# Kernel optimization log

Hardware: AMD Instinct MI355X
Metric: run time of the kernel (lower is better)

Reference implementation:

```python
import jax, jax.numpy as jnp
import numpy as np

DIM = 1024
HEADS = 16
DIM_HEAD = 64
INNER = HEADS * DIM_HEAD  # 1024
EPS = 1e-5


def setup_inputs() -> dict:
    key = jax.random.key(0)
    ks = jax.random.split(key, 5)
    x = jax.random.normal(ks[0], (4, 2048, DIM), dtype=jnp.float32)
    ln_gamma = jnp.ones((DIM,), dtype=jnp.float32)
    ln_beta = jnp.zeros((DIM,), dtype=jnp.float32)
    # nn.Linear weights ~ U(-1/sqrt(fan_in), 1/sqrt(fan_in)); stored as (out, in) in torch,
    # here kept as (in, out) for x @ W.
    lim = 1.0 / np.sqrt(DIM)
    w_qkv = jax.random.uniform(ks[1], (DIM, 3 * INNER), minval=-lim, maxval=lim, dtype=jnp.float32)
    lim2 = 1.0 / np.sqrt(INNER)
    w_out = jax.random.uniform(ks[2], (INNER, DIM), minval=-lim2, maxval=lim2, dtype=jnp.float32)
    return {"x": x, "ln_gamma": ln_gamma, "ln_beta": ln_beta, "w_qkv": w_qkv, "w_out": w_out}


def reference(x, ln_gamma, ln_beta, w_qkv, w_out):
    b, n, d = x.shape
    # LayerNorm
    mu = jnp.mean(x, axis=-1, keepdims=True)
    var = jnp.mean(jnp.square(x - mu), axis=-1, keepdims=True)
    xn = (x - mu) * jax.lax.rsqrt(var + EPS) * ln_gamma + ln_beta
    # QKV projection
    qkv = xn @ w_qkv  # (b, n, 3*inner)
    q, k, v = jnp.split(qkv, 3, axis=-1)
    def to_heads(t):
        return t.reshape(b, n, HEADS, DIM_HEAD).transpose(0, 2, 1, 3)  # (b,h,n,dh)
    q, k, v = to_heads(q), to_heads(k), to_heads(v)
    scale = DIM_HEAD ** -0.5
    scores = jnp.einsum('bhqd,bhkd->bhqk', q, k) * scale
    causal = jnp.tril(jnp.ones((n, n), dtype=bool))
    scores = jnp.where(causal, scores, -jnp.inf)
    probs = jax.nn.softmax(scores, axis=-1)
    out = jnp.einsum('bhqk,bhkd->bhqd', probs, v)
    out = out.transpose(0, 2, 1, 3).reshape(b, n, INNER)
    return out @ w_out
```

## Files before the change

kernel.cpp:

```cpp
#include <hip/hip_runtime.h>
#include <hip/hip_bf16.h>

#define DIM 1024
#define HEADS 16
#define DH 64
#define SEQ 2048
#define BATCH 4
#define ROWS (BATCH * SEQ)
#define NQKV (3 * DIM)

typedef __attribute__((ext_vector_type(8))) __bf16 bf16x8;
typedef __attribute__((ext_vector_type(4))) __bf16 bf16x4;
typedef __attribute__((ext_vector_type(4))) float f32x4;

__device__ inline void gload16(const void* g, void* l) {
  __builtin_amdgcn_global_load_lds(
      (const __attribute__((address_space(1))) void*)g,
      (__attribute__((address_space(3))) void*)l, 16, 0, 0);
}

__device__ inline float fast_exp2(float x) {
#if __has_builtin(__builtin_amdgcn_exp2f)
  return __builtin_amdgcn_exp2f(x);
#else
  return exp2f(x);
#endif
}

__global__ __launch_bounds__(256) void ln_kernel(
    const float* __restrict__ x, const float* __restrict__ gamma,
    const float* __restrict__ beta, __bf16* __restrict__ xnb) {
  const int row = blockIdx.x;
  const int tid = threadIdx.x;
  const float4* xr = (const float4*)(x + (size_t)row * DIM);
  float4 v = xr[tid];
  float s1 = v.x + v.y + v.z + v.w;
  float s2 = v.x * v.x + v.y * v.y + v.z * v.z + v.w * v.w;
#pragma unroll
  for (int d = 32; d > 0; d >>= 1) {
    s1 += __shfl_xor(s1, d);
    s2 += __shfl_xor(s2, d);
  }
  __shared__ float red1[4], red2[4];
  const int wave = tid >> 6, lane = tid & 63;
  if (lane == 0) { red1[wave] = s1; red2[wave] = s2; }
  __syncthreads();
  s1 = red1[0] + red1[1] + red1[2] + red1[3];
  s2 = red2[0] + red2[1] + red2[2] + red2[3];
  const float mean = s1 * (1.0f / DIM);
  const float var = s2 * (1.0f / DIM) - mean * mean;
  const float rstd = rsqrtf(var + 1e-5f);
  float4 g = ((const float4*)gamma)[tid];
  float4 b = ((const float4*)beta)[tid];
  bf16x4 o;
  o[0] = (__bf16)((v.x - mean) * rstd * g.x + b.x);
  o[1] = (__bf16)((v.y - mean) * rstd * g.y + b.y);
  o[2] = (__bf16)((v.z - mean) * rstd * g.z + b.z);
  o[3] = (__bf16)((v.w - mean) * rstd * g.w + b.w);
  *(bf16x4*)(xnb + (size_t)row * DIM + tid * 4) = o;
}

__global__ __launch_bounds__(256) void transpose_cast(
    const float* __restrict__ in, __bf16* __restrict__ outT, int rows, int cols) {
  __shared__ float tile[32][33];
  const int tx = threadIdx.x & 31, ty = threadIdx.x >> 5;
  const int c0 = blockIdx.x * 32, r0 = blockIdx.y * 32;
#pragma unroll
  for (int rr = ty; rr < 32; rr += 8)
    tile[rr][tx] = in[(size_t)(r0 + rr) * cols + c0 + tx];
  __syncthreads();
#pragma unroll
  for (int rr = ty; rr < 32; rr += 8)
    outT[(size_t)(c0 + rr) * rows + r0 + tx] = (__bf16)tile[tx][rr];
}

template <int MODE>
__global__ __launch_bounds__(256) void gemm128(
    const __bf16* __restrict__ A, const __bf16* __restrict__ Bt, int K, int N,
    float* __restrict__ Cout, __bf16* __restrict__ qb, __bf16* __restrict__ kb,
    __bf16* __restrict__ vtb) {
  __shared__ __bf16 As[2][128 * 32];
  __shared__ __bf16 Bs[2][128 * 32];
  const int tid = threadIdx.x;
  const int wave = tid >> 6, lane = tid & 63;
  const int quad = lane >> 4, l16 = lane & 15;
  const int wm = wave >> 1, wn = wave & 1;
  const size_t tileM = (size_t)blockIdx.x * 128;
  const size_t tileN = (size_t)blockIdx.y * 128;
  const int sel = (MODE == 1) ? (int)(tileN >> 10) : 0;
  const bool vmode = (MODE == 1) && (sel == 2);

  f32x4 acc[4][4];
#pragma unroll
  for (int i = 0; i < 4; ++i)
#pragma unroll
    for (int j = 0; j < 4; ++j) acc[i][j] = (f32x4){0.f, 0.f, 0.f, 0.f};

  const int sr = lane >> 2;
  const int sc = lane & 3;
  const int ck = (l16 >> 1) & 3;

  const __bf16* Abase = A + tileM * (size_t)K;
  const __bf16* Bbase = Bt + tileN * (size_t)K;

  auto stage = [&](int buf, int k0) {
#pragma unroll
    for (int p = 0; p < 2; ++p) {
      const int rbase = p * 64 + wave * 16;
      const int row = rbase + sr;
      const int gc = (sc ^ ((row >> 1) & 3)) << 3;
      gload16(Abase + (size_t)row * K + k0 + gc, &As[buf][rbase * 32]);
      gload16(Bbase + (size_t)row * K + k0 + gc, &Bs[buf][rbase * 32]);
    }
  };

  const int NIT = K >> 5;
  stage(0, 0);
  for (int it = 0; it < NIT; ++it) {
    __syncthreads();
    if (it + 1 < NIT) stage((it + 1) & 1, (it + 1) << 5);
    const int buf = it & 1;
    bf16x8 af[4], bfr[4];
#pragma unroll
    for (int mt = 0; mt < 4; ++mt)
      af[mt] =
          *(const bf16x8*)&As[buf][(wm * 64 + mt * 16 + l16) * 32 + ((quad ^ ck) << 3)];
#pragma unroll
    for (int nt = 0; nt < 4; ++nt)
      bfr[nt] =
          *(const bf16x8*)&Bs[buf][(wn * 64 + nt * 16 + l16) * 32 + ((quad ^ ck) << 3)];
    if (vmode) {
#pragma unroll
      for (int mt = 0; mt < 4; ++mt)
#pragma unroll
        for (int nt = 0; nt < 4; ++nt)
          acc[mt][nt] = __builtin_amdgcn_mfma_f32_16x16x32_bf16(af[mt], bfr[nt],
                                                                acc[mt][nt], 0, 0, 0);
    } else {
#pragma unroll
      for (int mt = 0; mt < 4; ++mt)
#pragma unroll
        for (int nt = 0; nt < 4; ++nt)
          acc[mt][nt] = __builtin_amdgcn_mfma_f32_16x16x32_bf16(bfr[nt], af[mt],
                                                                acc[mt][nt], 0, 0, 0);
    }
  }

  if (MODE == 0) {
#pragma unroll
    for (int mt = 0; mt < 4; ++mt) {
      const size_t m = tileM + wm * 64 + mt * 16 + l16;
#pragma unroll
      for (int nt = 0; nt < 4; ++nt) {
        const size_t n0 = tileN + wn * 64 + nt * 16 + quad * 4;
        *(f32x4*)&Cout[m * (size_t)N + n0] = acc[mt][nt];
      }
    }
  } else if (sel < 2) {
    __bf16* dst = (sel == 0) ? qb : kb;
#pragma unroll
    for (int mt = 0; mt < 4; ++mt) {
      const size_t m = tileM + wm * 64 + mt * 16 + l16;
      const int b = (int)(m >> 11), seq = (int)(m & 2047);
#pragma unroll
      for (int nt = 0; nt < 4; ++nt) {
        const int c = (int)(tileN & 1023) + wn * 64 + nt * 16 + quad * 4;
        const int head = c >> 6, dh = c & 63;
        bf16x4 pk;
#pragma unroll
        for (int r = 0; r < 4; ++r) pk[r] = (__bf16)acc[mt][nt][r];
        *(bf16x4*)&dst[(((size_t)b * HEADS + head) * SEQ + seq) * DH + dh] = pk;
      }
    }
  } else {
#pragma unroll
    for (int nt = 0; nt < 4; ++nt) {
      const int c = (int)(tileN & 1023) + wn * 64 + nt * 16 + l16;
      const int head = c >> 6, dh = c & 63;
#pragma unroll
      for (int mt = 0; mt < 4; ++mt) {
        const size_t m0 = tileM + wm * 64 + mt * 16 + quad * 4;
        const int b = (int)(m0 >> 11), seq = (int)(m0 & 2047);
        bf16x4 pk;
#pragma unroll
        for (int r = 0; r < 4; ++r) pk[r] = (__bf16)acc[mt][nt][r];
        *(bf16x4*)&vtb[(((size_t)b * HEADS + head) * DH + dh) * SEQ + seq] = pk;
      }
    }
  }
}

__global__ __launch_bounds__(256) void attn_kernel(
    const __bf16* __restrict__ qb, const __bf16* __restrict__ kb,
    const __bf16* __restrict__ vtb, __bf16* __restrict__ ob) {
  const int bh = blockIdx.x;
  const int bx = blockIdx.y;
  const int tid = threadIdx.x;
  const int wave = tid >> 6, lane = tid & 63;
  const int quad = lane >> 4, l16 = lane & 15;

  __shared__ __bf16 Ks[2][128 * 64];
  __shared__ __bf16 Vs[2][64 * 128];
  __shared__ __bf16 Ps[4][32 * 36];

  const __bf16* kg = kb + (size_t)bh * SEQ * DH;
  const __bf16* vg = vtb + (size_t)bh * DH * SEQ;

  const int i1 = bx, i2 = 15 - bx;
  const int T = 17;

  const int kr = lane >> 3, kc = lane & 7;
  const int vr = lane >> 4, vc = lane & 15;

  auto stage = [&](int buf, int j) {
#pragma unroll
    for (int p = 0; p < 4; ++p) {
      const int rbase = p * 32 + wave * 8;
      const int row = rbase + kr;
      gload16(kg + (size_t)(j * 128 + row) * DH + ((kc ^ (row & 7)) << 3),
              &Ks[buf][rbase * 64]);
    }
#pragma unroll
    for (int p = 0; p < 4; ++p) {
      const int rbase = p * 16 + wave * 4;
      const int row = rbase + vr;
      gload16(vg + (size_t)row * SEQ + j * 128 + ((vc ^ (row & 7)) << 3),
              &Vs[buf][rbase * 128]);
    }
  };

  const float QSCALE = 0.125f * 1.44269504088896f;
  bf16x8 qf[2][2];
  auto load_q = [&](int i) {
    const __bf16* qbase = qb + ((size_t)bh * SEQ + (size_t)i * 128 + wave * 32) * DH;
#pragma unroll
    for (int mt = 0; mt < 2; ++mt)
#pragma unroll
      for (int ks = 0; ks < 2; ++ks) {
        bf16x8 v = *(const bf16x8*)(qbase + (mt * 16 + l16) * DH + ks * 32 + quad * 8);
#pragma unroll
        for (int e = 0; e < 8; ++e) v[e] = (__bf16)((float)v[e] * QSCALE);
        qf[mt][ks] = v;
      }
  };

  float m_i[2], l_i[2];
  f32x4 o_acc[4][2];
  auto reset_state = [&]() {
#pragma unroll
    for (int mt = 0; mt < 2; ++mt) { m_i[mt] = -1e30f; l_i[mt] = 0.f; }
#pragma unroll
    for (int md = 0; md < 4; ++md)
#pragma unroll
      for (int mt = 0; mt < 2; ++mt) o_acc[md][mt] = (f32x4){0.f, 0.f, 0.f, 0.f};
  };
  const int b_out = bh >> 4, h_out = bh & 15;
  auto epilogue = [&](int i) {
#pragma unroll
    for (int mt = 0; mt < 2; ++mt) {
      float lsum = l_i[mt];
      lsum += __shfl_xor(lsum, 16);
      lsum += __shfl_xor(lsum, 32);
      const float inv = __builtin_amdgcn_rcpf(lsum);
      const int seq = i * 128 + wave * 32 + mt * 16 + l16;
      __bf16* dst = ob + ((size_t)b_out * SEQ + seq) * DIM + h_out * DH;
#pragma unroll
      for (int md = 0; md < 4; ++md) {
        bf16x4 pk;
#pragma unroll
        for (int r = 0; r < 4; ++r) pk[r] = (__bf16)(o_acc[md][mt][r] * inv);
        *(bf16x4*)(dst + md * 16 + quad * 4) = pk;
      }
    }
  };

  load_q(i1);
  reset_state();
  stage(0, 0);

  for (int t = 0; t < T; ++t) {
    __syncthreads();
    if (t + 1 < T) {
      const int jn = (t + 1 <= bx) ? (t + 1) : (t - bx);
      stage((t + 1) & 1, jn);
    }
    const int buf = t & 1;
    const int i = (t <= bx) ? i1 : i2;
    const int j = (t <= bx) ? t : (t - bx - 1);
    const bool diag = (j == i);

    f32x4 sa[8][2];
#pragma unroll
    for (int nt = 0; nt < 8; ++nt)
#pragma unroll
      for (int mt = 0; mt < 2; ++mt) sa[nt][mt] = (f32x4){0.f, 0.f, 0.f, 0.f};
#pragma unroll
    for (int nt = 0; nt < 8; ++nt)
#pragma unroll
      for (int ks = 0; ks < 2; ++ks) {
        bf16x8 kf = *(const bf16x8*)&Ks[buf][(nt * 16 + l16) * 64 +
                                            (((ks * 4 + quad) ^ (l16 & 7)) << 3)];
#pragma unroll
        for (int mt = 0; mt < 2; ++mt)
          sa[nt][mt] =
              __builtin_amdgcn_mfma_f32_16x16x32_bf16(kf, qf[mt][ks], sa[nt][mt], 0, 0, 0);
      }

    if (diag) {
#pragma unroll
      for (int nt = 0; nt < 8; ++nt)
#pragma unroll
        for (int mt = 0; mt < 2; ++mt) {
          const int qrow = wave * 32 + mt * 16 + l16;
#pragma unroll
          for (int r = 0; r < 4; ++r) {
            const int kv = nt * 16 + quad * 4 + r;
            if (kv > qrow) sa[nt][mt][r] = -1e30f;
          }
        }
    }

    float alpha[2];
#pragma unroll
    for (int mt = 0; mt < 2; ++mt) {
      float mx = -1e30f;
#pragma unroll
      for (int nt = 0; nt < 8; ++nt)
#pragma unroll
        for (int r = 0; r < 4; ++r) mx = fmaxf(mx, sa[nt][mt][r]);
      mx = fmaxf(mx, __shfl_xor(mx, 16));
      mx = fmaxf(mx, __shfl_xor(mx, 32));
      const float mnew = fmaxf(m_i[mt], mx);
      alpha[mt] = fast_exp2(m_i[mt] - mnew);
      m_i[mt] = mnew;
      float rs = 0.f;
#pragma unroll
      for (int nt = 0; nt < 8; ++nt)
#pragma unroll
        for (int r = 0; r < 4; ++r) {
          const float p = fast_exp2(sa[nt][mt][r] - mnew);
          sa[nt][mt][r] = p;
          rs += p;
        }
      l_i[mt] = l_i[mt] * alpha[mt] + rs;
    }
#pragma unroll
    for (int md = 0; md < 4; ++md)
#pragma unroll
      for (int mt = 0; mt < 2; ++mt)
#pragma unroll
        for (int r = 0; r < 4; ++r) o_acc[md][mt][r] *= alpha[mt];

#pragma unroll
    for (int c = 0; c < 4; ++c) {
#pragma unroll
      for (int mt = 0; mt < 2; ++mt)
#pragma unroll
        for (int ntl = 0; ntl < 2; ++ntl) {
          const int nt = c * 2 + ntl;
          bf16x4 pk;
#pragma unroll
          for (int r = 0; r < 4; ++r) pk[r] = (__bf16)sa[nt][mt][r];
          *(bf16x4*)&Ps[wave][(mt * 16 + l16) * 36 + ntl * 16 + quad * 4] = pk;
        }
      bf16x8 pf[2];
#pragma unroll
      for (int mt = 0; mt < 2; ++mt)
        pf[mt] = *(const bf16x8*)&Ps[wave][(mt * 16 + l16) * 36 + quad * 8];
#pragma unroll
      for (int md = 0; md < 4; ++md) {
        bf16x8 vf = *(const bf16x8*)&Vs[buf][(md * 16 + l16) * 128 +
                                            (((c * 4 + quad) ^ (l16 & 7)) << 3)];
#pragma unroll
        for (int mt = 0; mt < 2; ++mt)
          o_acc[md][mt] =
              __builtin_amdgcn_mfma_f32_16x16x32_bf16(vf, pf[mt], o_acc[md][mt], 0, 0, 0);
      }
    }

    if (t == bx) {
      epilogue(i1);
      reset_state();
      load_q(i2);
    }
  }
  epilogue(i2);
}

extern "C" void kernel_launch(void* const* d_in, const int* in_sizes, int n_in,
                              void* d_out, int out_size, void* d_ws, size_t ws_size,
                              hipStream_t stream) {
  const float* x = (const float*)d_in[0];
  const float* gamma = (const float*)d_in[1];
  const float* beta = (const float*)d_in[2];
  const float* w_qkv = (const float*)d_in[3];
  const float* w_out = (const float*)d_in[4];
  float* out = (float*)d_out;

  char* ws = (char*)d_ws;
  const size_t MB = 1024 * 1024;
  __bf16* xnb = (__bf16*)ws;
  __bf16* wqkvT = (__bf16*)(ws + 16 * MB);
  __bf16* woutT = (__bf16*)(ws + 24 * MB);
  __bf16* qbuf = (__bf16*)(ws + 32 * MB);
  __bf16* kbuf = (__bf16*)(ws + 48 * MB);
  __bf16* vtbuf = (__bf16*)(ws + 64 * MB);
  __bf16* attnb = xnb;

  ln_kernel<<<ROWS, 256, 0, stream>>>(x, gamma, beta, xnb);
  transpose_cast<<<dim3(NQKV / 32, DIM / 32), 256, 0, stream>>>(w_qkv, wqkvT, DIM, NQKV);
  transpose_cast<<<dim3(DIM / 32, DIM / 32), 256, 0, stream>>>(w_out, woutT, DIM, DIM);
  gemm128<1><<<dim3(ROWS / 128, NQKV / 128), 256, 0, stream>>>(
      xnb, wqkvT, DIM, NQKV, nullptr, qbuf, kbuf, vtbuf);
  attn_kernel<<<dim3(BATCH * HEADS, 8), 256, 0, stream>>>(qbuf, kbuf, vtbuf, attnb);
  gemm128<0><<<dim3(ROWS / 128, DIM / 128), 256, 0, stream>>>(
      attnb, woutT, DIM, DIM, out, nullptr, nullptr, nullptr);
}
```

Before: 316.2 us.

## Shrink attention tiles to 64x64 and double grid for occupancy

The attention kernel now uses 64-row query and 64-row KV tiles instead of 128, with each wave owning 16 query rows. The grid doubles to 16 paired row-blocks per head, and launch bounds request 4 blocks per CU. The aim is more blocks in flight, lower register and LDS use per block, and less wasted work on the causal diagonal. In exchange, each K/V tile loaded is reused by fewer query rows and there are more loop iterations with barriers.

```diff
diff --git a/kernel.cpp b/kernel.cpp
--- a/kernel.cpp
+++ b/kernel.cpp
@@ -190,87 +190,74 @@
   }
 }
 
-__global__ __launch_bounds__(256) void attn_kernel(
+__global__ __launch_bounds__(256, 4) void attn_kernel(
     const __bf16* __restrict__ qb, const __bf16* __restrict__ kb,
     const __bf16* __restrict__ vtb, __bf16* __restrict__ ob) {
   const int bh = blockIdx.x;
-  const int bx = blockIdx.y;
+  const int by = blockIdx.y;
   const int tid = threadIdx.x;
   const int wave = tid >> 6, lane = tid & 63;
   const int quad = lane >> 4, l16 = lane & 15;
 
-  __shared__ __bf16 Ks[2][128 * 64];
-  __shared__ __bf16 Vs[2][64 * 128];
-  __shared__ __bf16 Ps[4][32 * 36];
+  __shared__ __bf16 Ks[2][64 * 64];
+  __shared__ __bf16 Vs[2][64 * 64];
+  __shared__ __bf16 Ps[4][16 * 36];
 
   const __bf16* kg = kb + (size_t)bh * SEQ * DH;
   const __bf16* vg = vtb + (size_t)bh * DH * SEQ;
 
-  const int i1 = bx, i2 = 15 - bx;
-  const int T = 17;
+  const int i1 = by, i2 = 31 - by;
+  const int T = 33;
 
   const int kr = lane >> 3, kc = lane & 7;
-  const int vr = lane >> 4, vc = lane & 15;
 
   auto stage = [&](int buf, int j) {
 #pragma unroll
-    for (int p = 0; p < 4; ++p) {
-      const int rbase = p * 32 + wave * 8;
+    for (int p = 0; p < 2; ++p) {
+      const int rbase = wave * 16 + p * 8;
       const int row = rbase + kr;
-      gload16(kg + (size_t)(j * 128 + row) * DH + ((kc ^ (row & 7)) << 3),
+      gload16(kg + (size_t)(j * 64 + row) * DH + ((kc ^ (row & 7)) << 3),
               &Ks[buf][rbase * 64]);
-    }
-#pragma unroll
-    for (int p = 0; p < 4; ++p) {
-      const int rbase = p * 16 + wave * 4;
-      const int row = rbase + vr;
-      gload16(vg + (size_t)row * SEQ + j * 128 + ((vc ^ (row & 7)) << 3),
-              &Vs[buf][rbase * 128]);
+      gload16(vg + (size_t)row * SEQ + j * 64 + ((kc ^ (row & 7)) << 3),
+              &Vs[buf][rbase * 64]);
     }
   };
 
   const float QSCALE = 0.125f * 1.44269504088896f;
-  bf16x8 qf[2][2];
+  bf16x8 qf[2];
   auto load_q = [&](int i) {
-    const __bf16* qbase = qb + ((size_t)bh * SEQ + (size_t)i * 128 + wave * 32) * DH;
-#pragma unroll
-    for (int mt = 0; mt < 2; ++mt)
-#pragma unroll
-      for (int ks = 0; ks < 2; ++ks) {
-        bf16x8 v = *(const bf16x8*)(qbase + (mt * 16 + l16) * DH + ks * 32 + quad * 8);
-#pragma unroll
-        for (int e = 0; e < 8; ++e) v[e] = (__bf16)((float)v[e] * QSCALE);
-        qf[mt][ks] = v;
-      }
-  };
-
-  float m_i[2], l_i[2];
-  f32x4 o_acc[4][2];
+    const __bf16* qbase = qb + ((size_t)bh * SEQ + (size_t)i * 64 + wave * 16) * DH;
+#pragma unroll
+    for (int ks = 0; ks < 2; ++ks) {
+      bf16x8 v = *(const bf16x8*)(qbase + l16 * DH + ks * 32 + quad * 8);
+#pragma unroll
+      for (int e = 0; e < 8; ++e) v[e] = (__bf16)((float)v[e] * QSCALE);
+      qf[ks] = v;
+    }
+  };
+
+  float m_i, l_i;
+  f32x4 o_acc[4];
   auto reset_state = [&]() {
-#pragma unroll
-    for (int mt = 0; mt < 2; ++mt) { m_i[mt] = -1e30f; l_i[mt] = 0.f; }
-#pragma unroll
-    for (int md = 0; md < 4; ++md)
-#pragma unroll
-      for (int mt = 0; mt < 2; ++mt) o_acc[md][mt] = (f32x4){0.f, 0.f, 0.f, 0.f};
+    m_i = -1e30f;
+    l_i = 0.f;
+#pragma unroll
+    for (int md = 0; md < 4; ++md) o_acc[md] = (f32x4){0.f, 0.f, 0.f, 0.f};
   };
   const int b_out = bh >> 4, h_out = bh & 15;
   auto epilogue = [&](int i) {
-#pragma unroll
-    for (int mt = 0; mt < 2; ++mt) {
-      float lsum = l_i[mt];
-      lsum += __shfl_xor(lsum, 16);
-      lsum += __shfl_xor(lsum, 32);
-      const float inv = __builtin_amdgcn_rcpf(lsum);
-      const int seq = i * 128 + wave * 32 + mt * 16 + l16;
-      __bf16* dst = ob + ((size_t)b_out * SEQ + seq) * DIM + h_out * DH;
-#pragma unroll
-      for (int md = 0; md < 4; ++md) {
-        bf16x4 pk;
-#pragma unroll
-        for (int r = 0; r < 4; ++r) pk[r] = (__bf16)(o_acc[md][mt][r] * inv);
-        *(bf16x4*)(dst + md * 16 + quad * 4) = pk;
-      }
+    float lsum = l_i;
+    lsum += __shfl_xor(lsum, 16);
+    lsum += __shfl_xor(lsum, 32);
+    const float inv = __builtin_amdgcn_rcpf(lsum);
+    const int seq = i * 64 + wave * 16 + l16;
+    __bf16* dst = ob + ((size_t)b_out * SEQ + seq) * DIM + h_out * DH;
+#pragma unroll
+    for (int md = 0; md < 4; ++md) {
+      bf16x4 pk;
+#pragma unroll
+      for (int r = 0; r < 4; ++r) pk[r] = (__bf16)(o_acc[md][r] * inv);
+      *(bf16x4*)(dst + md * 16 + quad * 4) = pk;
     }
   };
 
@@ -281,104 +268,84 @@
   for (int t = 0; t < T; ++t) {
     __syncthreads();
     if (t + 1 < T) {
-      const int jn = (t + 1 <= bx) ? (t + 1) : (t - bx);
+      const int jn = (t + 1 <= by) ? (t + 1) : (t - by);
       stage((t + 1) & 1, jn);
     }
     const int buf = t & 1;
-    const int i = (t <= bx) ? i1 : i2;
-    const int j = (t <= bx) ? t : (t - bx - 1);
+    const int i = (t <= by) ? i1 : i2;
+    const int j = (t <= by) ? t : (t - by - 1);
     const bool diag = (j == i);
 
-    f32x4 sa[8][2];
-#pragma unroll
-    for (int nt = 0; nt < 8; ++nt)
-#pragma unroll
-      for (int mt = 0; mt < 2; ++mt) sa[nt][mt] = (f32x4){0.f, 0.f, 0.f, 0.f};
-#pragma unroll
-    for (int nt = 0; nt < 8; ++nt)
+    f32x4 sa[4];
+#pragma unroll
+    for (int nt = 0; nt < 4; ++nt) sa[nt] = (f32x4){0.f, 0.f, 0.f, 0.f};
+#pragma unroll
+    for (int nt = 0; nt < 4; ++nt)
 #pragma unroll
       for (int ks = 0; ks < 2; ++ks) {
         bf16x8 kf = *(const bf16x8*)&Ks[buf][(nt * 16 + l16) * 64 +
                                             (((ks * 4 + quad) ^ (l16 & 7)) << 3)];
-#pragma unroll
-        for (int mt = 0; mt < 2; ++mt)
-          sa[nt][mt] =
-              __builtin_amdgcn_mfma_f32_16x16x32_bf16(kf, qf[mt][ks], sa[nt][mt], 0, 0, 0);
+        sa[nt] = __builtin_amdgcn_mfma_f32_16x16x32_bf16(kf, qf[ks], sa[nt], 0, 0, 0);
       }
 
     if (diag) {
-#pragma unroll
-      for (int nt = 0; nt < 8; ++nt)
-#pragma unroll
-        for (int mt = 0; mt < 2; ++mt) {
-          const int qrow = wave * 32 + mt * 16 + l16;
-#pragma unroll
-          for (int r = 0; r < 4; ++r) {
-            const int kv = nt * 16 + quad * 4 + r;
-            if (kv > qrow) sa[nt][mt][r] = -1e30f;
-          }
+      const int qrl = wave * 16 + l16;
+#pragma unroll
+      for (int nt = 0; nt < 4; ++nt)
+#pragma unroll
+        for (int r = 0; r < 4; ++r) {
+          const int kvl = nt * 16 + quad * 4 + r;
+          if (kvl > qrl) sa[nt][r] = -1e30f;
         }
     }
 
-    float alpha[2];
-#pragma unroll
-    for (int mt = 0; mt < 2; ++mt) {
+    {
       float mx = -1e30f;
 #pragma unroll
-      for (int nt = 0; nt < 8; ++nt)
-#pragma unroll
-        for (int r = 0; r < 4; ++r) mx = fmaxf(mx, sa[nt][mt][r]);
+      for (int nt = 0; nt < 4; ++nt)
+#pragma unroll
+        for (int r = 0; r < 4; ++r) mx = fmaxf(mx, sa[nt][r]);
       mx = fmaxf(mx, __shfl_xor(mx, 16));
       mx = fmaxf(mx, __shfl_xor(mx, 32));
-      const float mnew = fmaxf(m_i[mt], mx);
-      alpha[mt] = fast_exp2(m_i[mt] - mnew);
-      m_i[mt] = mnew;
+      const float mnew = fmaxf(m_i, mx);
+      const float alpha = fast_exp2(m_i - mnew);
+      m_i = mnew;
       float rs = 0.f;
 #pragma unroll
-      for (int nt = 0; nt < 8; ++nt)
+      for (int nt = 0; nt < 4; ++nt)
 #pragma unroll
         for (int r = 0; r < 4; ++r) {
-          const float p = fast_exp2(sa[nt][mt][r] - mnew);
-          sa[nt][mt][r] = p;
+          const float p = fast_exp2(sa[nt][r] - mnew);
+          sa[nt][r] = p;
           rs += p;
         }
-      l_i[mt] = l_i[mt] * alpha[mt] + rs;
-    }
-#pragma unroll
-    for (int md = 0; md < 4; ++md)
-#pragma unroll
-      for (int mt = 0; mt < 2; ++mt)
-#pragma unroll
-        for (int r = 0; r < 4; ++r) o_acc[md][mt][r] *= alpha[mt];
-
-#pragma unroll
-    for (int c = 0; c < 4; ++c) {
-#pragma unroll
-      for (int mt = 0; mt < 2; ++mt)
-#pragma unroll
-        for (int ntl = 0; ntl < 2; ++ntl) {
-          const int nt = c * 2 + ntl;
-          bf16x4 pk;
-#pragma unroll
-          for (int r = 0; r < 4; ++r) pk[r] = (__bf16)sa[nt][mt][r];
-          *(bf16x4*)&Ps[wave][(mt * 16 + l16) * 36 + ntl * 16 + quad * 4] = pk;
-        }
-      bf16x8 pf[2];
-#pragma unroll
-      for (int mt = 0; mt < 2; ++mt)
-        pf[mt] = *(const bf16x8*)&Ps[wave][(mt * 16 + l16) * 36 + quad * 8];
+      l_i = l_i * alpha + rs;
+#pragma unroll
+      for (int md = 0; md < 4; ++md)
+#pragma unroll
+        for (int r = 0; r < 4; ++r) o_acc[md][r] *= alpha;
+    }
+
+#pragma unroll
+    for (int c = 0; c < 2; ++c) {
+#pragma unroll
+      for (int ntl = 0; ntl < 2; ++ntl) {
+        const int nt = c * 2 + ntl;
+        bf16x4 pk;
+#pragma unroll
+        for (int r = 0; r < 4; ++r) pk[r] = (__bf16)sa[nt][r];
+        *(bf16x4*)&Ps[wave][l16 * 36 + ntl * 16 + quad * 4] = pk;
+      }
+      bf16x8 pf = *(const bf16x8*)&Ps[wave][l16 * 36 + quad * 8];
 #pragma unroll
       for (int md = 0; md < 4; ++md) {
-        bf16x8 vf = *(const bf16x8*)&Vs[buf][(md * 16 + l16) * 128 +
+        bf16x8 vf = *(const bf16x8*)&Vs[buf][(md * 16 + l16) * 64 +
                                             (((c * 4 + quad) ^ (l16 & 7)) << 3)];
-#pragma unroll
-        for (int mt = 0; mt < 2; ++mt)
-          o_acc[md][mt] =
-              __builtin_amdgcn_mfma_f32_16x16x32_bf16(vf, pf[mt], o_acc[md][mt], 0, 0, 0);
-      }
-    }
-
-    if (t == bx) {
+        o_acc[md] = __builtin_amdgcn_mfma_f32_16x16x32_bf16(vf, pf, o_acc[md], 0, 0, 0);
+      }
+    }
+
+    if (t == by) {
       epilogue(i1);
       reset_state();
       load_q(i2);
@@ -412,7 +379,7 @@
   transpose_cast<<<dim3(DIM / 32, DIM / 32), 256, 0, stream>>>(w_out, woutT, DIM, DIM);
   gemm128<1><<<dim3(ROWS / 128, NQKV / 128), 256, 0, stream>>>(
       xnb, wqkvT, DIM, NQKV, nullptr, qbuf, kbuf, vtbuf);
-  attn_kernel<<<dim3(BATCH * HEADS, 8), 256, 0, stream>>>(qbuf, kbuf, vtbuf, attnb);
+  attn_kernel<<<dim3(BATCH * HEADS, 16), 256, 0, stream>>>(qbuf, kbuf, vtbuf, attnb);
   gemm128<0><<<dim3(ROWS / 128, DIM / 128), 256, 0, stream>>>(
       attnb, woutT, DIM, DIM, out, nullptr, nullptr, nullptr);
 }
```

New measurement: 287.0 us. 9.2% less time.
